# Performance work log

Hardware: AMD Instinct MI355X
Metric: run time of the kernel (lower is better)

The kernel has to match this reference:

```python
import jax, jax.numpy as jnp
import numpy as np

N, E, F_IN, E_IN, HID, H, C, L, OUT = 20000, 320000, 128, 64, 64, 4, 64, 4, 32


def setup_inputs() -> dict:
    key = jax.random.key(0)
    ks = jax.random.split(key, 24)
    s = 0.05
    return {
        'x': jax.random.normal(ks[0], (N, F_IN), jnp.float32),
        'edge_index': jax.random.randint(ks[1], (2, E), 0, N, jnp.int32),
        'edge_attr': jax.random.normal(ks[2], (E, E_IN), jnp.float32),
        'node_W': jax.random.normal(ks[3], (F_IN, HID), jnp.float32) * s,
        'node_b': jnp.zeros((HID,), jnp.float32),
        'eenc_W': jax.random.normal(ks[4], (E_IN, HID), jnp.float32) * s,
        'eenc_b': jnp.zeros((HID,), jnp.float32),
        'Wq': jax.random.normal(ks[5], (L, HID, H * C), jnp.float32) * s,
        'bq': jnp.zeros((L, H * C), jnp.float32),
        'Wk': jax.random.normal(ks[6], (L, HID, H * C), jnp.float32) * s,
        'bk': jnp.zeros((L, H * C), jnp.float32),
        'Wv': jax.random.normal(ks[7], (L, HID, H * C), jnp.float32) * s,
        'bv': jnp.zeros((L, H * C), jnp.float32),
        'We': jax.random.normal(ks[8], (L, HID, H * C), jnp.float32) * s,  # lin_edge, bias=False in PyG
        'Wskip': jax.random.normal(ks[9], (L, HID, HID), jnp.float32) * s,
        'bskip': jnp.zeros((L, HID), jnp.float32),
        'ln_g': jnp.ones((L, HID), jnp.float32),
        'ln_b': jnp.zeros((L, HID), jnp.float32),
        'lin_W': jax.random.normal(ks[10], (HID, OUT), jnp.float32) * s,
        'lin_b': jnp.zeros((OUT,), jnp.float32),
    }


def _layernorm(h, g, b):
    mu = h.mean(-1, keepdims=True)
    var = ((h - mu) ** 2).mean(-1, keepdims=True)
    return (h - mu) * jax.lax.rsqrt(var + 1e-5) * g + b


def _transformer_conv(h, ea, src, dst, Wq, bq, Wk, bk, Wv, bv, We, Wskip, bskip):
    n = h.shape[0]
    q = (h @ Wq + bq).reshape(n, H, C)[dst]          # [E,H,C] dst (x_i)
    k = (h @ Wk + bk).reshape(n, H, C)[src]          # [E,H,C] src (x_j)
    v = (h @ Wv + bv).reshape(n, H, C)[src]
    e = (ea @ We).reshape(-1, H, C)                  # per-edge features
    k = k + e
    alpha = (q * k).sum(-1) * (1.0 / jnp.sqrt(jnp.float32(C)))   # [E,H]
    amax = jax.ops.segment_max(alpha, dst, num_segments=n)       # segment softmax over dst
    ex = jnp.exp(alpha - amax[dst])
    denom = jax.ops.segment_sum(ex, dst, num_segments=n)
    a = ex / (denom[dst] + 1e-16)
    msg = (v + e) * a[..., None]                     # [E,H,C]
    out = jax.ops.segment_sum(msg, dst, num_segments=n)          # [N,H,C]
    out = out.mean(axis=1)                           # concat=False -> head mean
    return out + (h @ Wskip + bskip)                 # root_weight skip


def reference(x, edge_index, edge_attr, node_W, node_b, eenc_W, eenc_b,
              Wq, bq, Wk, bk, Wv, bv, We, Wskip, bskip, ln_g, ln_b, lin_W, lin_b):
    src, dst = edge_index[0], edge_index[1]
    h = x @ node_W + node_b
    ea = edge_attr @ eenc_W + eenc_b
    # layer 0: conv only (per the forward body)
    h = _transformer_conv(h, ea, src, dst, Wq[0], bq[0], Wk[0], bk[0], Wv[0], bv[0],
                          We[0], Wskip[0], bskip[0])
    # layers 1..L-1: res+ block (norm -> relu -> [dropout=id at eval] -> conv -> +res)
    for l in range(1, L):
        res = h
        z = _layernorm(h, ln_g[l], ln_b[l])
        z = jax.nn.relu(z)
        z = _transformer_conv(z, ea, src, dst, Wq[l], bq[l], Wk[l], bk[l], Wv[l], bv[l],
                              We[l], Wskip[l], bskip[l])
        h = z + res
    h = _layernorm(h, ln_g[0], ln_b[0])
    h = jax.nn.relu(h)
    return h @ lin_W + lin_b
```

## Files before the change

### kernel.cpp

```cpp
#include <hip/hip_runtime.h>
#include <hip/hip_fp16.h>
#include <math.h>

#define N_NODES 20000
#define N_EDGES 320000
#define F_IN    128
#define E_IN    64
#define HID     64
#define NH      4
#define CH      64
#define HC      256
#define L_LAYERS 4
#define OUT_DIM 32
#define WCOLS   1088

typedef _Float16 half8 __attribute__((ext_vector_type(8)));
typedef _Float16 half4 __attribute__((ext_vector_type(4)));
typedef float f32x4 __attribute__((ext_vector_type(4)));

__global__ __launch_bounds__(256) void hist_dst(const int* __restrict__ dst,
                                                int* __restrict__ hist) {
    int e = blockIdx.x * 256 + threadIdx.x;
    if (e < N_EDGES) atomicAdd(&hist[dst[e]], 1);
}

__global__ __launch_bounds__(1024) void build_order(const int* __restrict__ hist,
                                                    int* __restrict__ node_order,
                                                    int* __restrict__ rank_of,
                                                    int* __restrict__ deg_rank,
                                                    int* __restrict__ new_rp,
                                                    int* __restrict__ cursor2) {
    __shared__ int bins[256];
    __shared__ int curb[256];
    __shared__ int sums[1024];
    int t = threadIdx.x;
    if (t < 256) bins[t] = 0;
    __syncthreads();
    for (int n = t; n < N_NODES; n += 1024) {
        int d = hist[n]; if (d > 255) d = 255;
        atomicAdd(&bins[d], 1);
    }
    __syncthreads();
    if (t < 256) {
        int acc = 0;
        for (int b = t + 1; b < 256; b++) acc += bins[b];
        curb[t] = acc;
    }
    __syncthreads();
    for (int n = t; n < N_NODES; n += 1024) {
        int d = hist[n];
        int b = d > 255 ? 255 : d;
        int r = atomicAdd(&curb[b], 1);
        node_order[r] = n;
        rank_of[n] = r;
        deg_rank[r] = d;
    }
    __syncthreads();
    const int CHUNK = 20;
    int base = t * CHUNK;
    int local[CHUNK];
    int s = 0;
    for (int i = 0; i < CHUNK; i++) {
        int idx = base + i;
        int vv = (idx < N_NODES) ? deg_rank[idx] : 0;
        local[i] = s;
        s += vv;
    }
    sums[t] = s;
    __syncthreads();
    for (int off = 1; off < 1024; off <<= 1) {
        int v = (t >= off) ? sums[t - off] : 0;
        __syncthreads();
        sums[t] += v;
        __syncthreads();
    }
    int excl = (t == 0) ? 0 : sums[t - 1];
    for (int i = 0; i < CHUNK; i++) {
        int idx = base + i;
        if (idx < N_NODES) {
            int p = excl + local[i];
            new_rp[idx] = p;
            cursor2[idx] = p;
        }
    }
    if (t == 1023) new_rp[N_NODES] = sums[1023];
}

__global__ __launch_bounds__(256) void compute_pos(const int* __restrict__ src,
                                                   const int* __restrict__ dst,
                                                   const int* __restrict__ rank_of,
                                                   int* __restrict__ cursor2,
                                                   int* __restrict__ eid_of,
                                                   int* __restrict__ srcrank_perm) {
    int e = blockIdx.x * 256 + threadIdx.x;
    if (e >= N_EDGES) return;
    int r = rank_of[dst[e]];
    int pos = atomicAdd(&cursor2[r], 1);
    eid_of[pos] = e;
    srcrank_perm[pos] = rank_of[src[e]];
}

__global__ __launch_bounds__(256) void permute_attr(const int* __restrict__ eid_of,
                                                    const float* __restrict__ eattr,
                                                    __half* __restrict__ attr_p) {
    int t = threadIdx.x;
    int wave = t >> 6, lane = t & 63;
    int p = blockIdx.x * 16 + wave * 4 + (lane >> 4);
    if (p >= N_EDGES) return;
    int e = eid_of[p];
    int qi = (lane & 15) * 4;
    float4 a = *(const float4*)(eattr + (size_t)e * E_IN + qi);
    __half2 h0 = __floats2half2_rn(a.x, a.y);
    __half2 h1 = __floats2half2_rn(a.z, a.w);
    uint2 packed;
    packed.x = *(unsigned int*)&h0;
    packed.y = *(unsigned int*)&h1;
    *(uint2*)(attr_p + (size_t)p * E_IN + qi) = packed;
}

__global__ __launch_bounds__(256) void make_wqeA(const float* __restrict__ Wq,
                                                 const float* __restrict__ bq,
                                                 const float* __restrict__ We,
                                                 const float* __restrict__ eW,
                                                 const float* __restrict__ eb,
                                                 float* __restrict__ Wqe2,
                                                 float* __restrict__ bqe2,
                                                 float* __restrict__ wqb,
                                                 float* __restrict__ bqb) {
    int l = blockIdx.x / HID, i = blockIdx.x % HID;
    int t = threadIdx.x;
    int h = t >> 6, j = t & 63;
    __shared__ float wrow[256];
    __shared__ float brow[256];
    const float* WqL = Wq + (size_t)l * HID * HC;
    const float* WeL = We + (size_t)l * HID * HC;
    float acc = 0.f;
    for (int c = 0; c < CH; c++)
        acc += WqL[i * HC + h * CH + c] * WeL[j * HC + h * CH + c];
    wrow[t] = acc;
    if (i == 0) {
        const float* bqL = bq + l * HC;
        float ab = 0.f;
        for (int c = 0; c < CH; c++)
            ab += bqL[h * CH + c] * WeL[j * HC + h * CH + c];
        brow[t] = ab;
    }
    __syncthreads();
    int h2 = t >> 6, m = t & 63;
    float a2 = 0.f;
    for (int jj = 0; jj < HID; jj++) a2 += wrow[h2 * 64 + jj] * eW[m * HID + jj];
    Wqe2[(size_t)l * HID * HC + i * HC + t] = a2;
    if (m == 0) {
        float aw = 0.f;
        for (int jj = 0; jj < HID; jj++) aw += wrow[h2 * 64 + jj] * eb[jj];
        wqb[l * HID * NH + i * NH + h2] = aw;
    }
    if (i == 0) {
        float ab2 = 0.f;
        for (int jj = 0; jj < HID; jj++) ab2 += brow[h2 * 64 + jj] * eW[m * HID + jj];
        bqe2[l * HC + t] = ab2;
        if (m == 0) {
            float bb = 0.f;
            for (int jj = 0; jj < HID; jj++) bb += brow[h2 * 64 + jj] * eb[jj];
            bqb[l * NH + h2] = bb;
        }
    }
}

__global__ __launch_bounds__(256) void make_wcat(const float* __restrict__ eW,
                                                 const float* __restrict__ eb,
                                                 const float* __restrict__ We,
                                                 _Float16* __restrict__ Wcat16,
                                                 float* __restrict__ beE) {
    int l = blockIdx.x / 64, c = blockIdx.x % 64;
    int t = threadIdx.x;
    __shared__ float sh[4][64];
    {
        int j = t & 63, h = t >> 6;
        sh[h][j] = We[(size_t)l * HID * HC + j * HC + h * 64 + c];
    }
    __syncthreads();
    int h = t >> 6, m = t & 63;
    float acc = 0.f;
    for (int j = 0; j < HID; j++) acc += eW[m * HID + j] * sh[h][j];
    Wcat16[((size_t)l * 64 + c) * 256 + t] = (_Float16)acc;
    if (t < 4) {
        float a = 0.f;
        for (int j = 0; j < HID; j++) a += eb[j] * sh[t][j];
        beE[l * HC + t * 64 + c] = a;
    }
}

__global__ __launch_bounds__(256) void make_w16(
        const float* __restrict__ Wq, const float* __restrict__ Wk,
        const float* __restrict__ Wv, const float* __restrict__ Wqe2,
        const float* __restrict__ Wsk,
        const float* __restrict__ bq, const float* __restrict__ bk,
        const float* __restrict__ bv, const float* __restrict__ bqe2,
        const float* __restrict__ bsk,
        _Float16* __restrict__ W16T, float* __restrict__ biasc) {
    int l = blockIdx.x / 272;
    int cg = blockIdx.x % 272;
    int col = cg * 4 + (threadIdx.x >> 6);
    int i = threadIdx.x & 63;
    float w, b;
    if (col < 512) {
        int c = (col >> 3) * 4 + (col & 3);
        if ((col >> 2) & 1) { w = Wqe2[(size_t)l*HID*HC + i*HC + c]; b = bqe2[l*HC + c]; }
        else                { w = Wq[(size_t)l*HID*HC + i*HC + c];   b = bq[l*HC + c]; }
    } else if (col < 1024) {
        int cc = col - 512;
        int c = (cc >> 3) * 4 + (cc & 3);
        if ((cc >> 2) & 1) { w = Wv[(size_t)l*HID*HC + i*HC + c]; b = bv[l*HC + c]; }
        else               { w = Wk[(size_t)l*HID*HC + i*HC + c]; b = bk[l*HC + c]; }
    } else {
        int c = col - 1024;
        w = Wsk[(size_t)l*HID*HID + i*HID + c];  b = bsk[l*HID + c];
    }
    W16T[((size_t)l * WCOLS + col) * 64 + i] = (_Float16)w;
    if (i == 0) biasc[l * WCOLS + col] = b;
}

__global__ __launch_bounds__(256) void make_w0(const float* __restrict__ nW,
                                               const float* __restrict__ nb,
                                               _Float16* __restrict__ W0T,
                                               float* __restrict__ b0) {
    int col = blockIdx.x * 2 + (threadIdx.x >> 7);
    int i = threadIdx.x & 127;
    W0T[col * F_IN + i] = (_Float16)nW[i * HID + col];
    if (i == 0) b0[col] = nb[col];
}

__global__ __launch_bounds__(256) void node_pre0(const float* __restrict__ x,
        const int* __restrict__ node_order,
        const _Float16* __restrict__ W0T, const float* __restrict__ b0,
        const _Float16* __restrict__ W16T, const float* __restrict__ biasc,
        const float* __restrict__ wqb, const float* __restrict__ bqb,
        _Float16* __restrict__ qqw, _Float16* __restrict__ kv,
        float* __restrict__ skip, float* __restrict__ qb) {
    int t = threadIdx.x;
    int wave = t >> 6, lane = t & 63;
    int quad = lane >> 4, mrow = lane & 15;
    int base = blockIdx.x * 32;
    __shared__ _Float16 xs[32][136];
    __shared__ _Float16 zs[32][72];
    __shared__ int nord[32];
    if (t < 32) nord[t] = node_order[base + t];
    __syncthreads();
    for (int it = 0; it < 4; it++) {
        int idx = it * 256 + t;
        int m = idx >> 5, c4 = idx & 31;
        float4 a = *(const float4*)(x + (size_t)nord[m] * F_IN + c4 * 4);
        _Float16* d = &xs[m][c4 * 4];
        d[0] = (_Float16)a.x; d[1] = (_Float16)a.y;
        d[2] = (_Float16)a.z; d[3] = (_Float16)a.w;
    }
    __syncthreads();
    {
        int colb = wave * 16;
        const _Float16* w0row = W0T + (size_t)(colb + mrow) * F_IN;
        f32x4 acc0 = {0.f, 0.f, 0.f, 0.f};
        f32x4 acc1 = {0.f, 0.f, 0.f, 0.f};
#pragma unroll
        for (int kk = 0; kk < 4; kk++) {
            half8 wfrag = *(const half8*)(w0row + kk * 32 + quad * 8);
            half8 xf0 = *(const half8*)&xs[mrow][kk * 32 + quad * 8];
            half8 xf1 = *(const half8*)&xs[16 + mrow][kk * 32 + quad * 8];
            acc0 = __builtin_amdgcn_mfma_f32_16x16x32_f16(wfrag, xf0, acc0, 0, 0, 0);
            acc1 = __builtin_amdgcn_mfma_f32_16x16x32_f16(wfrag, xf1, acc1, 0, 0, 0);
        }
        float4 bb = *(const float4*)(b0 + colb + quad * 4);
        half4 h0v = {(_Float16)(acc0[0] + bb.x), (_Float16)(acc0[1] + bb.y),
                     (_Float16)(acc0[2] + bb.z), (_Float16)(acc0[3] + bb.w)};
        half4 h1v = {(_Float16)(acc1[0] + bb.x), (_Float16)(acc1[1] + bb.y),
                     (_Float16)(acc1[2] + bb.z), (_Float16)(acc1[3] + bb.w)};
        *(half4*)&zs[mrow][colb + quad * 4] = h0v;
        *(half4*)&zs[16 + mrow][colb + quad * 4] = h1v;
    }
    __syncthreads();
    {
        int p = t >> 1, s4 = t & 1;
        int m = p >> 2, h4 = p & 3;
        float a = 0.f;
        for (int i = s4 * 32; i < s4 * 32 + 32; i++)
            a += (float)zs[m][i] * wqb[i * NH + h4];
        a += __shfl_xor(a, 1);
        if (s4 == 0) qb[(base + m) * NH + h4] = a + bqb[h4];
    }
    half8 a00 = *(const half8*)&zs[mrow][quad * 8];
    half8 a01 = *(const half8*)&zs[mrow][32 + quad * 8];
    half8 a10 = *(const half8*)&zs[16 + mrow][quad * 8];
    half8 a11 = *(const half8*)&zs[16 + mrow][32 + quad * 8];
    int colwave = wave * 272;
    for (int tile = 0; tile < 17; tile++) {
        int colb = colwave + tile * 16;
        const _Float16* wrow = W16T + (size_t)(colb + mrow) * 64;
        half8 b0f = *(const half8*)(wrow + quad * 8);
        half8 b1f = *(const half8*)(wrow + 32 + quad * 8);
        f32x4 acc0 = {0.f, 0.f, 0.f, 0.f};
        f32x4 acc1 = {0.f, 0.f, 0.f, 0.f};
        acc0 = __builtin_amdgcn_mfma_f32_16x16x32_f16(b0f, a00, acc0, 0, 0, 0);
        acc0 = __builtin_amdgcn_mfma_f32_16x16x32_f16(b1f, a01, acc0, 0, 0, 0);
        acc1 = __builtin_amdgcn_mfma_f32_16x16x32_f16(b0f, a10, acc1, 0, 0, 0);
        acc1 = __builtin_amdgcn_mfma_f32_16x16x32_f16(b1f, a11, acc1, 0, 0, 0);
        float4 bi4 = *(const float4*)(biasc + colb + quad * 4);
        int wc = colb + quad * 4;
        int ra = base + mrow, rb = ra + 16;
        float v00 = acc0[0] + bi4.x, v01 = acc0[1] + bi4.y;
        float v02 = acc0[2] + bi4.z, v03 = acc0[3] + bi4.w;
        float v10 = acc1[0] + bi4.x, v11 = acc1[1] + bi4.y;
        float v12 = acc1[2] + bi4.z, v13 = acc1[3] + bi4.w;
        if (colb >= 1024) {
            *(float4*)(skip + ra * HID + (wc - 1024)) = make_float4(v00, v01, v02, v03);
            *(float4*)(skip + rb * HID + (wc - 1024)) = make_float4(v10, v11, v12, v13);
        } else {
            half4 p0 = {(_Float16)v00, (_Float16)v01, (_Float16)v02, (_Float16)v03};
            half4 p1 = {(_Float16)v10, (_Float16)v11, (_Float16)v12, (_Float16)v13};
            if (colb < 512) {
                *(half4*)(qqw + (size_t)ra * 512 + wc) = p0;
                *(half4*)(qqw + (size_t)rb * 512 + wc) = p1;
            } else {
                *(half4*)(kv + (size_t)ra * 512 + (wc - 512)) = p0;
                *(half4*)(kv + (size_t)rb * 512 + (wc - 512)) = p1;
            }
        }
    }
}

__global__ __launch_bounds__(256) void gather_edges(
        const int* __restrict__ new_rp,
        const int* __restrict__ srcrank_perm, const __half* __restrict__ attr_p,
        const __half* __restrict__ kv,
        const float* __restrict__ qb,
        const __half* qqw,
        float* numv, __half* __restrict__ numea16,
        float* __restrict__ den) {
    int wave = threadIdx.x >> 6;
    int lane = threadIdx.x & 63;
    int r = blockIdx.x * 4 + wave;
    if (r >= N_NODES) return;
    int e0 = new_rp[r], e1 = new_rp[r + 1];
    int qi = (lane & 15) * 4;
    int head = lane >> 4;
    uint4 qr = *(const uint4*)(qqw + (size_t)r * 512 + lane * 8);
    float2 q01 = __half22float2(*(__half2*)&qr.x);
    float2 q23 = __half22float2(*(__half2*)&qr.y);
    float2 w01 = __half22float2(*(__half2*)&qr.z);
    float2 w23 = __half22float2(*(__half2*)&qr.w);
    float qbh = qb[r * NH + head];
    float4 nv = make_float4(0.f, 0.f, 0.f, 0.f);
    float4 ne = make_float4(0.f, 0.f, 0.f, 0.f);
    float dsum = 0.f;
#pragma unroll 2
    for (int e = e0; e < e1; e++) {
        int s_ = srcrank_perm[e];
        uint2 araw = *(const uint2*)(attr_p + (size_t)e * E_IN + qi);
        uint4 kraw = *(const uint4*)(kv + (size_t)s_ * (2 * HC) + lane * 8);
        float2 a01 = __half22float2(*(__half2*)&araw.x);
        float2 a23 = __half22float2(*(__half2*)&araw.y);
        float2 k01 = __half22float2(*(__half2*)&kraw.x);
        float2 k23 = __half22float2(*(__half2*)&kraw.y);
        float2 v01 = __half22float2(*(__half2*)&kraw.z);
        float2 v23 = __half22float2(*(__half2*)&kraw.w);
        float rr = q01.x * k01.x + q01.y * k01.y + q23.x * k23.x + q23.y * k23.y
                 + w01.x * a01.x + w01.y * a01.y + w23.x * a23.x + w23.y * a23.y;
        rr += __shfl_xor(rr, 1);
        rr += __shfl_xor(rr, 2);
        rr += __shfl_xor(rr, 4);
        rr += __shfl_xor(rr, 8);
        float ex = __expf((rr + qbh) * 0.125f);
        nv.x += ex * v01.x; nv.y += ex * v01.y; nv.z += ex * v23.x; nv.w += ex * v23.y;
        ne.x += ex * a01.x; ne.y += ex * a01.y; ne.z += ex * a23.x; ne.w += ex * a23.y;
        dsum += ex;
    }
    *(float4*)(numv + (size_t)r * HC + lane * 4) = nv;
    __half2 n01 = __floats2half2_rn(ne.x, ne.y);
    __half2 n23 = __floats2half2_rn(ne.z, ne.w);
    uint2 np;
    np.x = *(unsigned int*)&n01;
    np.y = *(unsigned int*)&n23;
    *(uint2*)(numea16 + (size_t)r * HC + lane * 4) = np;
    if ((lane & 15) == 0) den[r * NH + head] = dsum;
}

__global__ __launch_bounds__(256) void node_mid(
        const float* numv,
        const __half* __restrict__ numea16,
        const float* __restrict__ den_g,
        float* skip,
        float* __restrict__ hg,
        const _Float16* __restrict__ Wcat16,
        const float* __restrict__ beE,
        int add_res,
        const _Float16* __restrict__ W16T,
        const float* __restrict__ biasc,
        const float* __restrict__ wqb, const float* __restrict__ bqb,
        const float* __restrict__ g, const float* __restrict__ be,
        _Float16* qqw, _Float16* __restrict__ kv,
        float* __restrict__ qb) {
    int t = threadIdx.x;
    int wave = t >> 6, lane = t & 63;
    int quad = lane >> 4, mrow = lane & 15;
    int base = blockIdx.x * 16;
    __shared__ _Float16 ea16[16][264];
    __shared__ float hnew[16][64];
    __shared__ _Float16 zs[16][72];
    __shared__ float bsh[256];
    __shared__ float rr_[64];
    __shared__ float ff_[64];
    if (t < 64) {
        float dd = den_g[base * 4 + t];
        float rc = 1.f / (dd + 1e-16f);
        rr_[t] = rc;
        ff_[t] = dd * rc;
    }
    bsh[t] = beE[t];
    __syncthreads();
    for (int it = 0; it < 2; it++) {
        int idx = it * 256 + t;
        int m = idx >> 5, c8 = idx & 31;
        float rc = rr_[m * 4 + (c8 >> 3)];
        uint4 raw = *(const uint4*)(numea16 + (size_t)(base + m) * HC + c8 * 8);
        __half2* hp = (__half2*)&raw;
#pragma unroll
        for (int i = 0; i < 4; i++) {
            float2 f = __half22float2(hp[i]);
            hp[i] = __floats2half2_rn(f.x * rc, f.y * rc);
        }
        *(uint4*)&ea16[m][c8 * 8] = raw;
    }
    __syncthreads();
    {
        int cb = wave * 16;
        f32x4 acc = {0.f, 0.f, 0.f, 0.f};
#pragma unroll
        for (int kk = 0; kk < 8; kk++) {
            half8 af = *(const half8*)&ea16[mrow][kk * 32 + quad * 8];
            half8 bf = *(const half8*)(Wcat16 + (size_t)(cb + mrow) * 256 + kk * 32 + quad * 8);
            acc = __builtin_amdgcn_mfma_f32_16x16x32_f16(af, bf, acc, 0, 0, 0);
        }
#pragma unroll
        for (int reg = 0; reg < 4; reg++)
            hnew[quad * 4 + reg][cb + mrow] = acc[reg];
    }
    __syncthreads();
    for (int it = 0; it < 4; it++) {
        int idx = it * 256 + t;
        int m = idx >> 6, c = idx & 63;
        float s = hnew[m][c];
#pragma unroll
        for (int hh = 0; hh < 4; hh++)
            s += numv[(size_t)(base + m) * HC + hh * 64 + c] * rr_[m * 4 + hh]
               + ff_[m * 4 + hh] * bsh[hh * 64 + c];
        s *= 0.25f;
        s += skip[(base + m) * HID + c];
        if (add_res) s += hg[(base + m) * HID + c];
        hg[(base + m) * HID + c] = s;
        hnew[m][c] = s;
    }
    __syncthreads();
    for (int it = 0; it < 4; it++) {
        int m = it * 4 + wave;
        float val = hnew[m][lane];
        float mu = val;
        for (int o = 32; o > 0; o >>= 1) mu += __shfl_xor(mu, o);
        mu *= (1.f / 64.f);
        float d = val - mu;
        float var = d * d;
        for (int o = 32; o > 0; o >>= 1) var += __shfl_xor(var, o);
        var *= (1.f / 64.f);
        val = fmaxf(d * rsqrtf(var + 1e-5f) * g[lane] + be[lane], 0.f);
        zs[m][lane] = (_Float16)val;
    }
    __syncthreads();
    {
        int p = t >> 2, s4 = t & 3;
        int m = p >> 2, h4 = p & 3;
        float a = 0.f;
        for (int i = s4 * 16; i < s4 * 16 + 16; i++)
            a += (float)zs[m][i] * wqb[i * NH + h4];
        a += __shfl_xor(a, 1);
        a += __shfl_xor(a, 2);
        if (s4 == 0) qb[(base + m) * NH + h4] = a + bqb[h4];
    }
    half8 a00 = *(const half8*)&zs[mrow][quad * 8];
    half8 a01 = *(const half8*)&zs[mrow][32 + quad * 8];
    int colwave = wave * 272;
    for (int tile = 0; tile < 17; tile++) {
        int colb = colwave + tile * 16;
        const _Float16* wrow = W16T + (size_t)(colb + mrow) * 64;
        half8 b0f = *(const half8*)(wrow + quad * 8);
        half8 b1f = *(const half8*)(wrow + 32 + quad * 8);
        f32x4 acc = {0.f, 0.f, 0.f, 0.f};
        acc = __builtin_amdgcn_mfma_f32_16x16x32_f16(b0f, a00, acc, 0, 0, 0);
        acc = __builtin_amdgcn_mfma_f32_16x16x32_f16(b1f, a01, acc, 0, 0, 0);
        float4 bi4 = *(const float4*)(biasc + colb + quad * 4);
        int wc = colb + quad * 4;
        int ra = base + mrow;
        float v0 = acc[0] + bi4.x, v1 = acc[1] + bi4.y;
        float v2 = acc[2] + bi4.z, v3 = acc[3] + bi4.w;
        if (colb >= 1024) {
            *(float4*)(skip + ra * HID + (wc - 1024)) = make_float4(v0, v1, v2, v3);
        } else {
            half4 pk = {(_Float16)v0, (_Float16)v1, (_Float16)v2, (_Float16)v3};
            if (colb < 512) *(half4*)(qqw + (size_t)ra * 512 + wc) = pk;
            else            *(half4*)(kv + (size_t)ra * 512 + (wc - 512)) = pk;
        }
    }
}

__global__ __launch_bounds__(256) void node_fin(
        const int* __restrict__ node_order,
        const float* __restrict__ numv,
        const __half* __restrict__ numea16,
        const float* __restrict__ den_g,
        const float* __restrict__ skip,
        const float* __restrict__ hg,
        const _Float16* __restrict__ Wcat16, const float* __restrict__ beE,
        const float* __restrict__ g, const float* __restrict__ be,
        const float* __restrict__ linW, const float* __restrict__ linb,
        float* __restrict__ out) {
    int t = threadIdx.x;
    int wave = t >> 6, lane = t & 63;
    int quad = lane >> 4, mrow = lane & 15;
    int base = blockIdx.x * 16;
    __shared__ _Float16 ea16[16][264];
    __shared__ float hnew[16][64];
    __shared__ float bsh[256];
    __shared__ float rr_[64];
    __shared__ float ff_[64];
    __shared__ int nord[16];
    if (t < 16) nord[t] = node_order[base + t];
    if (t < 64) {
        float dd = den_g[base * 4 + t];
        float rc = 1.f / (dd + 1e-16f);
        rr_[t] = rc;
        ff_[t] = dd * rc;
    }
    bsh[t] = beE[t];
    __syncthreads();
    for (int it = 0; it < 2; it++) {
        int idx = it * 256 + t;
        int m = idx >> 5, c8 = idx & 31;
        float rc = rr_[m * 4 + (c8 >> 3)];
        uint4 raw = *(const uint4*)(numea16 + (size_t)(base + m) * HC + c8 * 8);
        __half2* hp = (__half2*)&raw;
#pragma unroll
        for (int i = 0; i < 4; i++) {
            float2 f = __half22float2(hp[i]);
            hp[i] = __floats2half2_rn(f.x * rc, f.y * rc);
        }
        *(uint4*)&ea16[m][c8 * 8] = raw;
    }
    __syncthreads();
    {
        int cb = wave * 16;
        f32x4 acc = {0.f, 0.f, 0.f, 0.f};
#pragma unroll
        for (int kk = 0; kk < 8; kk++) {
            half8 af = *(const half8*)&ea16[mrow][kk * 32 + quad * 8];
            half8 bf = *(const half8*)(Wcat16 + (size_t)(cb + mrow) * 256 + kk * 32 + quad * 8);
            acc = __builtin_amdgcn_mfma_f32_16x16x32_f16(af, bf, acc, 0, 0, 0);
        }
#pragma unroll
        for (int reg = 0; reg < 4; reg++)
            hnew[quad * 4 + reg][cb + mrow] = acc[reg];
    }
    __syncthreads();
    for (int it = 0; it < 4; it++) {
        int idx = it * 256 + t;
        int m = idx >> 6, c = idx & 63;
        float s = hnew[m][c];
#pragma unroll
        for (int hh = 0; hh < 4; hh++)
            s += numv[(size_t)(base + m) * HC + hh * 64 + c] * rr_[m * 4 + hh]
               + ff_[m * 4 + hh] * bsh[hh * 64 + c];
        s *= 0.25f;
        s += skip[(base + m) * HID + c] + hg[(base + m) * HID + c];
        hnew[m][c] = s;
    }
    __syncthreads();
    for (int it = 0; it < 4; it++) {
        int m = it * 4 + wave;
        float val = hnew[m][lane];
        float mu = val;
        for (int o = 32; o > 0; o >>= 1) mu += __shfl_xor(mu, o);
        mu *= (1.f / 64.f);
        float d = val - mu;
        float var = d * d;
        for (int o = 32; o > 0; o >>= 1) var += __shfl_xor(var, o);
        var *= (1.f / 64.f);
        hnew[m][lane] = fmaxf(d * rsqrtf(var + 1e-5f) * g[lane] + be[lane], 0.f);
    }
    __syncthreads();
    for (int it = 0; it < 2; it++) {
        int idx = it * 256 + t;
        int m = idx >> 5, col = idx & 31;
        float a = linb[col];
        for (int i = 0; i < HID; i++) a += hnew[m][i] * linW[i * OUT_DIM + col];
        out[nord[m] * OUT_DIM + col] = a;
    }
}

extern "C" void kernel_launch(void* const* d_in, const int* in_sizes, int n_in,
                              void* d_out, int out_size, void* d_ws, size_t ws_size,
                              hipStream_t stream) {
    const float* x      = (const float*)d_in[0];
    const int*   ei     = (const int*)d_in[1];
    const float* eattr  = (const float*)d_in[2];
    const float* node_W = (const float*)d_in[3];
    const float* node_b = (const float*)d_in[4];
    const float* eenc_W = (const float*)d_in[5];
    const float* eenc_b = (const float*)d_in[6];
    const float* Wq     = (const float*)d_in[7];
    const float* bq     = (const float*)d_in[8];
    const float* Wk     = (const float*)d_in[9];
    const float* bk     = (const float*)d_in[10];
    const float* Wv     = (const float*)d_in[11];
    const float* bv     = (const float*)d_in[12];
    const float* We     = (const float*)d_in[13];
    const float* Wskip  = (const float*)d_in[14];
    const float* bskip  = (const float*)d_in[15];
    const float* ln_g   = (const float*)d_in[16];
    const float* ln_b   = (const float*)d_in[17];
    const float* lin_W  = (const float*)d_in[18];
    const float* lin_b  = (const float*)d_in[19];
    float* out = (float*)d_out;

    const int* src = ei;
    const int* dst = ei + N_EDGES;

    float* ws = (float*)d_ws;
    __half* attr_p = (__half*)ws; ws += (size_t)N_EDGES * E_IN / 2;
    float* h    = ws; ws += N_NODES * HID;
    _Float16* qqw = (_Float16*)ws; ws += (size_t)N_NODES * HC;
    float* numv = (float*)qqw;
    __half* numea16 = (__half*)ws; ws += (size_t)N_NODES * HC / 2;
    _Float16* kv = (_Float16*)ws; ws += (size_t)N_NODES * HC;
    float* skip = ws; ws += N_NODES * HID;
    float* den  = ws; ws += N_NODES * NH;
    float* qb   = ws; ws += N_NODES * NH;
    float* Wqe2 = ws; ws += (size_t)L_LAYERS * HID * HC;
    float* bqe2 = ws; ws += L_LAYERS * HC;
    float* wqb  = ws; ws += L_LAYERS * HID * NH;
    float* bqb  = ws; ws += L_LAYERS * NH;
    _Float16* Wcat16 = (_Float16*)ws; ws += (size_t)L_LAYERS * 64 * 256 / 2;
    float* beE  = ws; ws += L_LAYERS * HC;
    _Float16* W16T = (_Float16*)ws; ws += (size_t)L_LAYERS * WCOLS * HID / 2;
    float* biasc = ws; ws += L_LAYERS * WCOLS;
    _Float16* W0T = (_Float16*)ws; ws += HID * F_IN / 2;
    float* b0  = ws; ws += HID;
    int* ip = (int*)ws;
    int* hist         = ip; ip += N_NODES;
    int* node_order   = ip; ip += N_NODES;
    int* rank_of      = ip; ip += N_NODES;
    int* deg_rank     = ip; ip += N_NODES;
    int* new_rp       = ip; ip += N_NODES + 4;
    int* cursor2      = ip; ip += N_NODES;
    int* srcrank_perm = ip; ip += N_EDGES;
    int* eid_of       = ip; ip += N_EDGES;

    hipMemsetAsync(hist, 0, N_NODES * sizeof(int), stream);
    hist_dst<<<(N_EDGES + 255) / 256, 256, 0, stream>>>(dst, hist);
    build_order<<<1, 1024, 0, stream>>>(hist, node_order, rank_of, deg_rank,
                                        new_rp, cursor2);

    make_wqeA<<<L_LAYERS * HID, 256, 0, stream>>>(Wq, bq, We, eenc_W, eenc_b,
                                                  Wqe2, bqe2, wqb, bqb);
    make_wcat<<<L_LAYERS * 64, 256, 0, stream>>>(eenc_W, eenc_b, We, Wcat16, beE);
    make_w16<<<L_LAYERS * 272, 256, 0, stream>>>(Wq, Wk, Wv, Wqe2, Wskip,
                                                 bq, bk, bv, bqe2, bskip,
                                                 W16T, biasc);
    make_w0<<<HID / 2, 256, 0, stream>>>(node_W, node_b, W0T, b0);

    compute_pos<<<(N_EDGES + 255) / 256, 256, 0, stream>>>(src, dst, rank_of, cursor2,
                                                           eid_of, srcrank_perm);
    permute_attr<<<N_EDGES / 16, 256, 0, stream>>>(eid_of, eattr, attr_p);

    node_pre0<<<N_NODES / 32, 256, 0, stream>>>(
        x, node_order, W0T, b0, W16T, biasc, wqb, bqb, qqw, kv, skip, qb);

    for (int l = 0; l < L_LAYERS; l++) {
        gather_edges<<<(N_NODES + 3) / 4, 256, 0, stream>>>(
            new_rp, srcrank_perm, attr_p, (const __half*)kv, qb,
            (const __half*)qqw, numv, numea16, den);
        if (l < L_LAYERS - 1) {
            node_mid<<<N_NODES / 16, 256, 0, stream>>>(
                numv, numea16, den, skip, h,
                Wcat16 + (size_t)l * 64 * 256, beE + l * HC,
                (l > 0) ? 1 : 0,
                W16T + (size_t)(l + 1) * WCOLS * HID, biasc + (l + 1) * WCOLS,
                wqb + (l + 1) * HID * NH, bqb + (l + 1) * NH,
                ln_g + (l + 1) * HID, ln_b + (l + 1) * HID,
                qqw, kv, qb);
        } else {
            node_fin<<<N_NODES / 16, 256, 0, stream>>>(
                node_order, numv, numea16, den, skip, h,
                Wcat16 + (size_t)l * 64 * 256, beE + l * HC,
                ln_g, ln_b, lin_W, lin_b, out);
        }
    }
}
```

Before: 674.4 us.

## Fuse edge gather with node update into a single per-layer kernel

Merges the per-destination edge gather and the node update/projection kernels (mid and final) into one layer_step kernel. Per-node softmax numerators are normalised in registers and staged in shared memory instead of being written to and re-read from global numv/numea16/den buffers. The kv buffer is double-buffered because other blocks still read source rows during the layer. Blocks now cover 8 nodes, with each wave handling 2 nodes in sequence, so half of each 16-row MFMA tile is wasted and there are fewer independent gather waves in flight. The value numerator is also kept in fp16 rather than fp32.

```diff
diff --git a/kernel.cpp b/kernel.cpp
--- a/kernel.cpp
+++ b/kernel.cpp
@@ -327,107 +327,83 @@
     }
 }
 
-__global__ __launch_bounds__(256) void gather_edges(
+__global__ __launch_bounds__(256) void layer_step(
         const int* __restrict__ new_rp,
-        const int* __restrict__ srcrank_perm, const __half* __restrict__ attr_p,
-        const __half* __restrict__ kv,
-        const float* __restrict__ qb,
-        const __half* qqw,
-        float* numv, __half* __restrict__ numea16,
-        float* __restrict__ den) {
-    int wave = threadIdx.x >> 6;
-    int lane = threadIdx.x & 63;
-    int r = blockIdx.x * 4 + wave;
-    if (r >= N_NODES) return;
-    int e0 = new_rp[r], e1 = new_rp[r + 1];
-    int qi = (lane & 15) * 4;
-    int head = lane >> 4;
-    uint4 qr = *(const uint4*)(qqw + (size_t)r * 512 + lane * 8);
-    float2 q01 = __half22float2(*(__half2*)&qr.x);
-    float2 q23 = __half22float2(*(__half2*)&qr.y);
-    float2 w01 = __half22float2(*(__half2*)&qr.z);
-    float2 w23 = __half22float2(*(__half2*)&qr.w);
-    float qbh = qb[r * NH + head];
-    float4 nv = make_float4(0.f, 0.f, 0.f, 0.f);
-    float4 ne = make_float4(0.f, 0.f, 0.f, 0.f);
-    float dsum = 0.f;
-#pragma unroll 2
-    for (int e = e0; e < e1; e++) {
-        int s_ = srcrank_perm[e];
-        uint2 araw = *(const uint2*)(attr_p + (size_t)e * E_IN + qi);
-        uint4 kraw = *(const uint4*)(kv + (size_t)s_ * (2 * HC) + lane * 8);
-        float2 a01 = __half22float2(*(__half2*)&araw.x);
-        float2 a23 = __half22float2(*(__half2*)&araw.y);
-        float2 k01 = __half22float2(*(__half2*)&kraw.x);
-        float2 k23 = __half22float2(*(__half2*)&kraw.y);
-        float2 v01 = __half22float2(*(__half2*)&kraw.z);
-        float2 v23 = __half22float2(*(__half2*)&kraw.w);
-        float rr = q01.x * k01.x + q01.y * k01.y + q23.x * k23.x + q23.y * k23.y
-                 + w01.x * a01.x + w01.y * a01.y + w23.x * a23.x + w23.y * a23.y;
-        rr += __shfl_xor(rr, 1);
-        rr += __shfl_xor(rr, 2);
-        rr += __shfl_xor(rr, 4);
-        rr += __shfl_xor(rr, 8);
-        float ex = __expf((rr + qbh) * 0.125f);
-        nv.x += ex * v01.x; nv.y += ex * v01.y; nv.z += ex * v23.x; nv.w += ex * v23.y;
-        ne.x += ex * a01.x; ne.y += ex * a01.y; ne.z += ex * a23.x; ne.w += ex * a23.y;
-        dsum += ex;
-    }
-    *(float4*)(numv + (size_t)r * HC + lane * 4) = nv;
-    __half2 n01 = __floats2half2_rn(ne.x, ne.y);
-    __half2 n23 = __floats2half2_rn(ne.z, ne.w);
-    uint2 np;
-    np.x = *(unsigned int*)&n01;
-    np.y = *(unsigned int*)&n23;
-    *(uint2*)(numea16 + (size_t)r * HC + lane * 4) = np;
-    if ((lane & 15) == 0) den[r * NH + head] = dsum;
-}
-
-__global__ __launch_bounds__(256) void node_mid(
-        const float* numv,
-        const __half* __restrict__ numea16,
-        const float* __restrict__ den_g,
-        float* skip,
+        const int* __restrict__ srcrank_perm,
+        const __half* __restrict__ attr_p,
+        const __half* __restrict__ kv_in,
+        _Float16* __restrict__ qqw,
+        float* __restrict__ qb,
+        float* __restrict__ skip,
         float* __restrict__ hg,
-        const _Float16* __restrict__ Wcat16,
-        const float* __restrict__ beE,
+        const _Float16* __restrict__ Wcat16, const float* __restrict__ beE,
         int add_res,
-        const _Float16* __restrict__ W16T,
-        const float* __restrict__ biasc,
+        const _Float16* __restrict__ W16T, const float* __restrict__ biasc,
         const float* __restrict__ wqb, const float* __restrict__ bqb,
         const float* __restrict__ g, const float* __restrict__ be,
-        _Float16* qqw, _Float16* __restrict__ kv,
-        float* __restrict__ qb) {
+        _Float16* __restrict__ kv_out,
+        int last,
+        const int* __restrict__ node_order,
+        const float* __restrict__ linW, const float* __restrict__ linb,
+        float* __restrict__ out) {
     int t = threadIdx.x;
     int wave = t >> 6, lane = t & 63;
     int quad = lane >> 4, mrow = lane & 15;
-    int base = blockIdx.x * 16;
+    int head = quad;
+    int base = blockIdx.x * 8;
     __shared__ _Float16 ea16[16][264];
-    __shared__ float hnew[16][64];
+    __shared__ _Float16 nvs[8][264];
+    __shared__ float hnew[8][64];
     __shared__ _Float16 zs[16][72];
     __shared__ float bsh[256];
-    __shared__ float rr_[64];
-    __shared__ float ff_[64];
-    if (t < 64) {
-        float dd = den_g[base * 4 + t];
-        float rc = 1.f / (dd + 1e-16f);
-        rr_[t] = rc;
-        ff_[t] = dd * rc;
-    }
+    __shared__ float ffs[32];
+    __shared__ int nord[8];
     bsh[t] = beE[t];
-    __syncthreads();
-    for (int it = 0; it < 2; it++) {
-        int idx = it * 256 + t;
-        int m = idx >> 5, c8 = idx & 31;
-        float rc = rr_[m * 4 + (c8 >> 3)];
-        uint4 raw = *(const uint4*)(numea16 + (size_t)(base + m) * HC + c8 * 8);
-        __half2* hp = (__half2*)&raw;
-#pragma unroll
-        for (int i = 0; i < 4; i++) {
-            float2 f = __half22float2(hp[i]);
-            hp[i] = __floats2half2_rn(f.x * rc, f.y * rc);
-        }
-        *(uint4*)&ea16[m][c8 * 8] = raw;
+    if (t < 8) nord[t] = node_order[base + t];
+    int qi = mrow * 4;
+    for (int rep = 0; rep < 2; rep++) {
+        int m = wave * 2 + rep;
+        int r = base + m;
+        int e0 = new_rp[r], e1 = new_rp[r + 1];
+        uint4 qr = *(const uint4*)(qqw + (size_t)r * 512 + lane * 8);
+        float2 q01 = __half22float2(*(__half2*)&qr.x);
+        float2 q23 = __half22float2(*(__half2*)&qr.y);
+        float2 w01 = __half22float2(*(__half2*)&qr.z);
+        float2 w23 = __half22float2(*(__half2*)&qr.w);
+        float qbh = qb[r * NH + head];
+        float4 nv = make_float4(0.f, 0.f, 0.f, 0.f);
+        float4 ne = make_float4(0.f, 0.f, 0.f, 0.f);
+        float dsum = 0.f;
+#pragma unroll 2
+        for (int e = e0; e < e1; e++) {
+            int s_ = srcrank_perm[e];
+            uint2 araw = *(const uint2*)(attr_p + (size_t)e * E_IN + qi);
+            uint4 kraw = *(const uint4*)(kv_in + (size_t)s_ * 512 + lane * 8);
+            float2 a01 = __half22float2(*(__half2*)&araw.x);
+            float2 a23 = __half22float2(*(__half2*)&araw.y);
+            float2 k01 = __half22float2(*(__half2*)&kraw.x);
+            float2 k23 = __half22float2(*(__half2*)&kraw.y);
+            float2 v01 = __half22float2(*(__half2*)&kraw.z);
+            float2 v23 = __half22float2(*(__half2*)&kraw.w);
+            float rr = q01.x * k01.x + q01.y * k01.y + q23.x * k23.x + q23.y * k23.y
+                     + w01.x * a01.x + w01.y * a01.y + w23.x * a23.x + w23.y * a23.y;
+            rr += __shfl_xor(rr, 1);
+            rr += __shfl_xor(rr, 2);
+            rr += __shfl_xor(rr, 4);
+            rr += __shfl_xor(rr, 8);
+            float ex = __expf((rr + qbh) * 0.125f);
+            nv.x += ex * v01.x; nv.y += ex * v01.y; nv.z += ex * v23.x; nv.w += ex * v23.y;
+            ne.x += ex * a01.x; ne.y += ex * a01.y; ne.z += ex * a23.x; ne.w += ex * a23.y;
+            dsum += ex;
+        }
+        float rc = 1.f / (dsum + 1e-16f);
+        half4 nep = {(_Float16)(ne.x * rc), (_Float16)(ne.y * rc),
+                     (_Float16)(ne.z * rc), (_Float16)(ne.w * rc)};
+        half4 nvp = {(_Float16)(nv.x * rc), (_Float16)(nv.y * rc),
+                     (_Float16)(nv.z * rc), (_Float16)(nv.w * rc)};
+        *(half4*)&ea16[m][lane * 4] = nep;
+        *(half4*)&nvs[m][lane * 4] = nvp;
+        if (mrow == 0) ffs[m * 4 + head] = dsum * rc;
     }
     __syncthreads();
     {
@@ -439,27 +415,28 @@
             half8 bf = *(const half8*)(Wcat16 + (size_t)(cb + mrow) * 256 + kk * 32 + quad * 8);
             acc = __builtin_amdgcn_mfma_f32_16x16x32_f16(af, bf, acc, 0, 0, 0);
         }
+        if (quad < 2) {
 #pragma unroll
-        for (int reg = 0; reg < 4; reg++)
-            hnew[quad * 4 + reg][cb + mrow] = acc[reg];
-    }
-    __syncthreads();
-    for (int it = 0; it < 4; it++) {
+            for (int reg = 0; reg < 4; reg++)
+                hnew[quad * 4 + reg][cb + mrow] = acc[reg];
+        }
+    }
+    __syncthreads();
+    for (int it = 0; it < 2; it++) {
         int idx = it * 256 + t;
         int m = idx >> 6, c = idx & 63;
         float s = hnew[m][c];
 #pragma unroll
         for (int hh = 0; hh < 4; hh++)
-            s += numv[(size_t)(base + m) * HC + hh * 64 + c] * rr_[m * 4 + hh]
-               + ff_[m * 4 + hh] * bsh[hh * 64 + c];
+            s += (float)nvs[m][hh * 64 + c] + ffs[m * 4 + hh] * bsh[hh * 64 + c];
         s *= 0.25f;
         s += skip[(base + m) * HID + c];
         if (add_res) s += hg[(base + m) * HID + c];
-        hg[(base + m) * HID + c] = s;
+        if (!last) hg[(base + m) * HID + c] = s;
         hnew[m][c] = s;
     }
     __syncthreads();
-    for (int it = 0; it < 4; it++) {
+    for (int it = 0; it < 2; it++) {
         int m = it * 4 + wave;
         float val = hnew[m][lane];
         float mu = val;
@@ -470,18 +447,27 @@
         for (int o = 32; o > 0; o >>= 1) var += __shfl_xor(var, o);
         var *= (1.f / 64.f);
         val = fmaxf(d * rsqrtf(var + 1e-5f) * g[lane] + be[lane], 0.f);
-        zs[m][lane] = (_Float16)val;
-    }
-    __syncthreads();
+        if (last) hnew[m][lane] = val;
+        else      zs[m][lane] = (_Float16)val;
+    }
+    __syncthreads();
+    if (last) {
+        int m = t >> 5, col = t & 31;
+        float a = linb[col];
+        for (int i = 0; i < HID; i++) a += hnew[m][i] * linW[i * OUT_DIM + col];
+        out[nord[m] * OUT_DIM + col] = a;
+        return;
+    }
     {
-        int p = t >> 2, s4 = t & 3;
+        int p = t >> 3, s8 = t & 7;
         int m = p >> 2, h4 = p & 3;
         float a = 0.f;
-        for (int i = s4 * 16; i < s4 * 16 + 16; i++)
+        for (int i = s8 * 8; i < s8 * 8 + 8; i++)
             a += (float)zs[m][i] * wqb[i * NH + h4];
         a += __shfl_xor(a, 1);
         a += __shfl_xor(a, 2);
-        if (s4 == 0) qb[(base + m) * NH + h4] = a + bqb[h4];
+        a += __shfl_xor(a, 4);
+        if (s8 == 0) qb[(base + m) * NH + h4] = a + bqb[h4];
     }
     half8 a00 = *(const half8*)&zs[mrow][quad * 8];
     half8 a01 = *(const half8*)&zs[mrow][32 + quad * 8];
@@ -494,111 +480,20 @@
         f32x4 acc = {0.f, 0.f, 0.f, 0.f};
         acc = __builtin_amdgcn_mfma_f32_16x16x32_f16(b0f, a00, acc, 0, 0, 0);
         acc = __builtin_amdgcn_mfma_f32_16x16x32_f16(b1f, a01, acc, 0, 0, 0);
-        float4 bi4 = *(const float4*)(biasc + colb + quad * 4);
-        int wc = colb + quad * 4;
-        int ra = base + mrow;
-        float v0 = acc[0] + bi4.x, v1 = acc[1] + bi4.y;
-        float v2 = acc[2] + bi4.z, v3 = acc[3] + bi4.w;
-        if (colb >= 1024) {
-            *(float4*)(skip + ra * HID + (wc - 1024)) = make_float4(v0, v1, v2, v3);
-        } else {
-            half4 pk = {(_Float16)v0, (_Float16)v1, (_Float16)v2, (_Float16)v3};
-            if (colb < 512) *(half4*)(qqw + (size_t)ra * 512 + wc) = pk;
-            else            *(half4*)(kv + (size_t)ra * 512 + (wc - 512)) = pk;
-        }
-    }
-}
-
-__global__ __launch_bounds__(256) void node_fin(
-        const int* __restrict__ node_order,
-        const float* __restrict__ numv,
-        const __half* __restrict__ numea16,
-        const float* __restrict__ den_g,
-        const float* __restrict__ skip,
-        const float* __restrict__ hg,
-        const _Float16* __restrict__ Wcat16, const float* __restrict__ beE,
-        const float* __restrict__ g, const float* __restrict__ be,
-        const float* __restrict__ linW, const float* __restrict__ linb,
-        float* __restrict__ out) {
-    int t = threadIdx.x;
-    int wave = t >> 6, lane = t & 63;
-    int quad = lane >> 4, mrow = lane & 15;
-    int base = blockIdx.x * 16;
-    __shared__ _Float16 ea16[16][264];
-    __shared__ float hnew[16][64];
-    __shared__ float bsh[256];
-    __shared__ float rr_[64];
-    __shared__ float ff_[64];
-    __shared__ int nord[16];
-    if (t < 16) nord[t] = node_order[base + t];
-    if (t < 64) {
-        float dd = den_g[base * 4 + t];
-        float rc = 1.f / (dd + 1e-16f);
-        rr_[t] = rc;
-        ff_[t] = dd * rc;
-    }
-    bsh[t] = beE[t];
-    __syncthreads();
-    for (int it = 0; it < 2; it++) {
-        int idx = it * 256 + t;
-        int m = idx >> 5, c8 = idx & 31;
-        float rc = rr_[m * 4 + (c8 >> 3)];
-        uint4 raw = *(const uint4*)(numea16 + (size_t)(base + m) * HC + c8 * 8);
-        __half2* hp = (__half2*)&raw;
-#pragma unroll
-        for (int i = 0; i < 4; i++) {
-            float2 f = __half22float2(hp[i]);
-            hp[i] = __floats2half2_rn(f.x * rc, f.y * rc);
-        }
-        *(uint4*)&ea16[m][c8 * 8] = raw;
-    }
-    __syncthreads();
-    {
-        int cb = wave * 16;
-        f32x4 acc = {0.f, 0.f, 0.f, 0.f};
-#pragma unroll
-        for (int kk = 0; kk < 8; kk++) {
-            half8 af = *(const half8*)&ea16[mrow][kk * 32 + quad * 8];
-            half8 bf = *(const half8*)(Wcat16 + (size_t)(cb + mrow) * 256 + kk * 32 + quad * 8);
-            acc = __builtin_amdgcn_mfma_f32_16x16x32_f16(af, bf, acc, 0, 0, 0);
-        }
-#pragma unroll
-        for (int reg = 0; reg < 4; reg++)
-            hnew[quad * 4 + reg][cb + mrow] = acc[reg];
-    }
-    __syncthreads();
-    for (int it = 0; it < 4; it++) {
-        int idx = it * 256 + t;
-        int m = idx >> 6, c = idx & 63;
-        float s = hnew[m][c];
-#pragma unroll
-        for (int hh = 0; hh < 4; hh++)
-            s += numv[(size_t)(base + m) * HC + hh * 64 + c] * rr_[m * 4 + hh]
-               + ff_[m * 4 + hh] * bsh[hh * 64 + c];
-        s *= 0.25f;
-        s += skip[(base + m) * HID + c] + hg[(base + m) * HID + c];
-        hnew[m][c] = s;
-    }
-    __syncthreads();
-    for (int it = 0; it < 4; it++) {
-        int m = it * 4 + wave;
-        float val = hnew[m][lane];
-        float mu = val;
-        for (int o = 32; o > 0; o >>= 1) mu += __shfl_xor(mu, o);
-        mu *= (1.f / 64.f);
-        float d = val - mu;
-        float var = d * d;
-        for (int o = 32; o > 0; o >>= 1) var += __shfl_xor(var, o);
-        var *= (1.f / 64.f);
-        hnew[m][lane] = fmaxf(d * rsqrtf(var + 1e-5f) * g[lane] + be[lane], 0.f);
-    }
-    __syncthreads();
-    for (int it = 0; it < 2; it++) {
-        int idx = it * 256 + t;
-        int m = idx >> 5, col = idx & 31;
-        float a = linb[col];
-        for (int i = 0; i < HID; i++) a += hnew[m][i] * linW[i * OUT_DIM + col];
-        out[nord[m] * OUT_DIM + col] = a;
+        if (mrow < 8) {
+            float4 bi4 = *(const float4*)(biasc + colb + quad * 4);
+            int wc = colb + quad * 4;
+            int ra = base + mrow;
+            float v0 = acc[0] + bi4.x, v1 = acc[1] + bi4.y;
+            float v2 = acc[2] + bi4.z, v3 = acc[3] + bi4.w;
+            if (colb >= 1024) {
+                *(float4*)(skip + ra * HID + (wc - 1024)) = make_float4(v0, v1, v2, v3);
+            } else {
+                half4 pk = {(_Float16)v0, (_Float16)v1, (_Float16)v2, (_Float16)v3};
+                if (colb < 512) *(half4*)(qqw + (size_t)ra * 512 + wc) = pk;
+                else            *(half4*)(kv_out + (size_t)ra * 512 + (wc - 512)) = pk;
+            }
+        }
     }
 }
 
@@ -634,11 +529,9 @@
     __half* attr_p = (__half*)ws; ws += (size_t)N_EDGES * E_IN / 2;
     float* h    = ws; ws += N_NODES * HID;
     _Float16* qqw = (_Float16*)ws; ws += (size_t)N_NODES * HC;
-    float* numv = (float*)qqw;
-    __half* numea16 = (__half*)ws; ws += (size_t)N_NODES * HC / 2;
-    _Float16* kv = (_Float16*)ws; ws += (size_t)N_NODES * HC;
+    _Float16* kvA = (_Float16*)ws; ws += (size_t)N_NODES * HC;
+    _Float16* kvB = (_Float16*)ws; ws += (size_t)N_NODES * HC;
     float* skip = ws; ws += N_NODES * HID;
-    float* den  = ws; ws += N_NODES * NH;
     float* qb   = ws; ws += N_NODES * NH;
     float* Wqe2 = ws; ws += (size_t)L_LAYERS * HID * HC;
     float* bqe2 = ws; ws += L_LAYERS * HC;
@@ -678,26 +571,22 @@
     permute_attr<<<N_EDGES / 16, 256, 0, stream>>>(eid_of, eattr, attr_p);
 
     node_pre0<<<N_NODES / 32, 256, 0, stream>>>(
-        x, node_order, W0T, b0, W16T, biasc, wqb, bqb, qqw, kv, skip, qb);
+        x, node_order, W0T, b0, W16T, biasc, wqb, bqb, qqw, kvA, skip, qb);
 
     for (int l = 0; l < L_LAYERS; l++) {
-        gather_edges<<<(N_NODES + 3) / 4, 256, 0, stream>>>(
-            new_rp, srcrank_perm, attr_p, (const __half*)kv, qb,
-            (const __half*)qqw, numv, numea16, den);
-        if (l < L_LAYERS - 1) {
-            node_mid<<<N_NODES / 16, 256, 0, stream>>>(
-                numv, numea16, den, skip, h,
-                Wcat16 + (size_t)l * 64 * 256, beE + l * HC,
-                (l > 0) ? 1 : 0,
-                W16T + (size_t)(l + 1) * WCOLS * HID, biasc + (l + 1) * WCOLS,
-                wqb + (l + 1) * HID * NH, bqb + (l + 1) * NH,
-                ln_g + (l + 1) * HID, ln_b + (l + 1) * HID,
-                qqw, kv, qb);
-        } else {
-            node_fin<<<N_NODES / 16, 256, 0, stream>>>(
-                node_order, numv, numea16, den, skip, h,
-                Wcat16 + (size_t)l * 64 * 256, beE + l * HC,
-                ln_g, ln_b, lin_W, lin_b, out);
-        }
-    }
-}
+        const _Float16* kin = (l & 1) ? kvB : kvA;
+        _Float16* kout = (l & 1) ? kvA : kvB;
+        int last = (l == L_LAYERS - 1);
+        int lnext = last ? 0 : (l + 1);
+        layer_step<<<N_NODES / 8, 256, 0, stream>>>(
+            new_rp, srcrank_perm, attr_p, (const __half*)kin,
+            qqw, qb, skip, h,
+            Wcat16 + (size_t)l * 64 * 256, beE + l * HC,
+            (l > 0) ? 1 : 0,
+            W16T + (size_t)lnext * WCOLS * HID, biasc + lnext * WCOLS,
+            wqb + lnext * HID * NH, bqb + lnext * NH,
+            last ? ln_g : (ln_g + (l + 1) * HID),
+            last ? ln_b : (ln_b + (l + 1) * HID),
+            kout, last, node_order, lin_W, lin_b, out);
+    }
+}
```

New measurement: 754.8 us. 11.9% more time.
